# Kernel optimization log

Hardware: AMD Instinct MI355X
Metric: run time of the kernel (lower is better)

Reference implementation:

```python
import jax, jax.numpy as jnp
import numpy as np

NEG_BIG = -9e15  # matches torch's -9000000000000000.0 mask value


def _gat_layer(x, adj_mask, W, a):
    # x: [N, Fin], W: [Fin, Fout], a: [Fout]
    h = x @ W                                   # [N, Fout]
    d = jnp.abs(h[None, :, :] - h[:, None, :])  # [N, N, Fout] pairwise |h_j - h_i|
    e = jax.nn.relu(jnp.einsum('ijf,f->ij', d, a))
    e = jnp.where(adj_mask, e, NEG_BIG)
    att = jax.nn.softmax(e, axis=1)             # row softmax (dropout p=0, skipped)
    return jax.nn.relu(att @ h)


def setup_inputs() -> dict:
    key = jax.random.key(0)
    ks = jax.random.split(key, 10)
    N, F, H, C = 1024, 128, 128, 16

    def xavier(k, shape, gain=1.414):
        fan_in, fan_out = shape[0], shape[-1]
        bound = gain * np.sqrt(6.0 / (fan_in + fan_out))
        return jax.random.uniform(k, shape, jnp.float32, -bound, bound)

    feat = jax.random.normal(ks[0], (N, F), jnp.float32)
    adj = jax.random.randint(ks[1], (N, N), 0, 2, jnp.int32)
    return {
        'feat': feat,
        'adj': adj,
        'W1': xavier(ks[2], (F, H)), 'a1': xavier(ks[3], (H, 1)).squeeze(-1),
        'W2': xavier(ks[4], (H, H)), 'a2': xavier(ks[5], (H, 1)).squeeze(-1),
        'W3': xavier(ks[6], (H, H)), 'a3': xavier(ks[7], (H, 1)).squeeze(-1),
        'Wfc': xavier(ks[8], (H, C), gain=1.0),
        'bfc': jnp.zeros((C,), jnp.float32),
    }


def reference(feat, adj, W1, a1, W2, a2, W3, a3, Wfc, bfc):
    mask = adj > 0
    x = _gat_layer(feat, mask, W1, a1)
    x = _gat_layer(x, mask, W2, a2)
    x = _gat_layer(x, mask, W3, a3)
    # EdgeGCN (include_adj=False): pairwise abs-diff -> linear, output [N*N, C]
    N, H = x.shape
    diff = jnp.abs(x[None, :, :] - x[:, None, :]).reshape(N * N, H)
    return diff @ Wfc + bfc
```

## Files before the change

kernel.cpp:

```cpp
#include <hip/hip_runtime.h>
#include <math.h>

#define NEG_BIG -9.0e15f

typedef __attribute__((ext_vector_type(4))) float f32x4;
typedef __attribute__((ext_vector_type(8))) short bf16x8;
typedef __attribute__((ext_vector_type(4))) unsigned int u32x4;

__global__ __launch_bounds__(128) void gemm_xw_t(const float* __restrict__ X,
                                                 const float* __restrict__ W,
                                                 float* __restrict__ HT) {
  __shared__ float xrow[128];
  const int i = blockIdx.x;
  const int o = threadIdx.x;
  xrow[o] = X[(size_t)i * 128 + o];
  __syncthreads();
  float acc = 0.f;
#pragma unroll 16
  for (int k = 0; k < 128; ++k) acc = fmaf(xrow[k], W[(size_t)k * 128 + o], acc);
  HT[(size_t)o * 1024 + i] = acc;
}

#define ABSFMA4(acc, hv, ha)                        \
  acc.x = fmaf(fabsf(hv.x - ha.x), ha.y, acc.x);    \
  acc.y = fmaf(fabsf(hv.y - ha.x), ha.y, acc.y);    \
  acc.z = fmaf(fabsf(hv.z - ha.x), ha.y, acc.z);    \
  acc.w = fmaf(fabsf(hv.w - ha.x), ha.y, acc.w);

#define DOT4(acc, hv, p) \
  acc = fmaf(hv.x, p.x, fmaf(hv.y, p.y, fmaf(hv.z, p.z, fmaf(hv.w, p.w, acc))));

__global__ __launch_bounds__(1024, 4) void gat_attn(const float* __restrict__ HT,
                                                    const int* __restrict__ adj,
                                                    const float* __restrict__ a,
                                                    float* __restrict__ Xout) {
  __shared__ float ep2[2][4][1024];
  __shared__ float e_s[4][1024];
  __shared__ float2 ha_s[4][128];
  __shared__ float redm[4][4];
  __shared__ float redsum[4][4];
  __shared__ float inv_s[4];

  const int t = threadIdx.x;
  const int i0 = blockIdx.x * 4;
  const float4* __restrict__ HT4 = reinterpret_cast<const float4*>(HT);

  if (t < 512) {
    const int pil = t >> 7;
    const int f = t & 127;
    ha_s[pil][f] = make_float2(HT[(size_t)f * 1024 + i0 + pil], a[f]);
  }
  __syncthreads();

  const int ih = t >> 9;
  const int fh = (t >> 8) & 1;
  const int jt = t & 255;
  const int il = t >> 8;
  const int j0 = (t & 255) * 4;

  float4 esum = {0.f, 0.f, 0.f, 0.f};
#pragma unroll
  for (int pass = 0; pass < 2; ++pass) {
    const int fb = pass * 64 + fh * 32;
    float4 aA = {0.f, 0.f, 0.f, 0.f};
    float4 aB = {0.f, 0.f, 0.f, 0.f};
#pragma unroll 4
    for (int ff = 0; ff < 32; ++ff) {
      const int f = fb + ff;
      const float4 hv = HT4[f * 256 + jt];
      const float2 hA = ha_s[ih * 2][f];
      const float2 hB = ha_s[ih * 2 + 1][f];
      ABSFMA4(aA, hv, hA);
      ABSFMA4(aB, hv, hB);
    }
    *reinterpret_cast<float4*>(&ep2[fh][ih * 2][jt * 4]) = aA;
    *reinterpret_cast<float4*>(&ep2[fh][ih * 2 + 1][jt * 4]) = aB;
    __syncthreads();
    {
      const float4 s0 = *reinterpret_cast<const float4*>(&ep2[0][il][j0]);
      const float4 s1 = *reinterpret_cast<const float4*>(&ep2[1][il][j0]);
      esum.x += s0.x + s1.x;
      esum.y += s0.y + s1.y;
      esum.z += s0.z + s1.z;
      esum.w += s0.w + s1.w;
    }
    __syncthreads();
  }

  float4 e;
  {
    const int4 ad = *reinterpret_cast<const int4*>(&adj[(size_t)(i0 + il) * 1024 + j0]);
    e.x = ad.x > 0 ? fmaxf(esum.x, 0.f) : NEG_BIG;
    e.y = ad.y > 0 ? fmaxf(esum.y, 0.f) : NEG_BIG;
    e.z = ad.z > 0 ? fmaxf(esum.z, 0.f) : NEG_BIG;
    e.w = ad.w > 0 ? fmaxf(esum.w, 0.f) : NEG_BIG;
  }

  const int wq = (t >> 6) & 3;
  float m = fmaxf(fmaxf(e.x, e.y), fmaxf(e.z, e.w));
#pragma unroll
  for (int off = 32; off > 0; off >>= 1) m = fmaxf(m, __shfl_xor(m, off));
  if ((t & 63) == 0) redm[il][wq] = m;
  __syncthreads();
  m = fmaxf(fmaxf(redm[il][0], redm[il][1]), fmaxf(redm[il][2], redm[il][3]));
  float4 p;
  p.x = __expf(e.x - m);
  p.y = __expf(e.y - m);
  p.z = __expf(e.z - m);
  p.w = __expf(e.w - m);
  *reinterpret_cast<float4*>(&e_s[il][j0]) = p;
  float s = p.x + p.y + p.z + p.w;
#pragma unroll
  for (int off = 32; off > 0; off >>= 1) s += __shfl_xor(s, off);
  if ((t & 63) == 0) redsum[il][wq] = s;
  __syncthreads();
  if (t < 4) {
    const float ss = redsum[t][0] + redsum[t][1] + redsum[t][2] + redsum[t][3];
    inv_s[t] = 1.f / ss;
  }
  __syncthreads();

  const int w = t >> 6;
  const int l = t & 63;
  const int f0 = w * 8;
  float acc[8][4];
#pragma unroll
  for (int ff = 0; ff < 8; ++ff)
#pragma unroll
    for (int r = 0; r < 4; ++r) acc[ff][r] = 0.f;

#pragma unroll
  for (int jb = 0; jb < 4; ++jb) {
    const int j4 = jb * 64 + l;
    const float4 p0 = *reinterpret_cast<const float4*>(&e_s[0][j4 * 4]);
    const float4 p1 = *reinterpret_cast<const float4*>(&e_s[1][j4 * 4]);
    const float4 p2 = *reinterpret_cast<const float4*>(&e_s[2][j4 * 4]);
    const float4 p3 = *reinterpret_cast<const float4*>(&e_s[3][j4 * 4]);
#pragma unroll
    for (int ff = 0; ff < 8; ++ff) {
      const float4 hv = HT4[(f0 + ff) * 256 + j4];
      DOT4(acc[ff][0], hv, p0);
      DOT4(acc[ff][1], hv, p1);
      DOT4(acc[ff][2], hv, p2);
      DOT4(acc[ff][3], hv, p3);
    }
  }

  float v[32];
#pragma unroll
  for (int ff = 0; ff < 8; ++ff)
#pragma unroll
    for (int r = 0; r < 4; ++r) v[ff * 4 + r] = acc[ff][r];

#pragma unroll
  for (int step = 0; step < 5; ++step) {
    const int s2 = 1 << step;
    const bool hi = (l & s2) != 0;
#pragma unroll
    for (int k = 0; k < (32 >> (step + 1)); ++k) {
      const float x = v[2 * k];
      const float y = v[2 * k + 1];
      float tt = hi ? x : y;
      tt = __shfl_xor(tt, s2);
      v[k] = (hi ? y : x) + tt;
    }
  }
  float r = v[0] + __shfl_xor(v[0], 32);

  if (l < 32) {
    const int oidx = l & 31;
    const int ff = oidx >> 2;
    const int orow = oidx & 3;
    const float o = fmaxf(r * inv_s[orow], 0.f);
    Xout[(size_t)(i0 + orow) * 128 + f0 + ff] = o;
  }
}

__global__ __launch_bounds__(256) void edge_fc_mfma(const float* __restrict__ X,
                                                    const float* __restrict__ Wfc,
                                                    const float* __restrict__ bfc,
                                                    float* __restrict__ out) {
  __shared__ float xi_s[32][132];
  __shared__ float xj_s[32][132];
  __shared__ float ostage[4][256];

  const int t = threadIdx.x;
  const int bid = blockIdx.x;
  int jb = (int)((sqrtf(8.0f * (float)bid + 1.0f) - 1.0f) * 0.5f);
  int ib = bid - jb * (jb + 1) / 2;
  if (ib > jb) { jb++; ib = bid - jb * (jb + 1) / 2; }
  if (ib < 0) { jb--; ib = bid - jb * (jb + 1) / 2; }

  {
    const int r = t >> 3;
    const int c0 = (t & 7) * 16;
    const float4* gi = reinterpret_cast<const float4*>(X + (size_t)(ib * 32 + r) * 128 + c0);
    const float4* gj = reinterpret_cast<const float4*>(X + (size_t)(jb * 32 + r) * 128 + c0);
#pragma unroll
    for (int k = 0; k < 4; ++k) {
      *reinterpret_cast<float4*>(&xi_s[r][c0 + k * 4]) = gi[k];
      *reinterpret_cast<float4*>(&xj_s[r][c0 + k * 4]) = gj[k];
    }
  }

  const int w = t >> 6, lane = t & 63;
  const int col = lane & 15, kg = lane >> 4;

  bf16x8 bhi[4], blo[4];
#pragma unroll
  for (int c = 0; c < 4; ++c) {
    bf16x8 bh, bl;
#pragma unroll
    for (int j = 0; j < 8; ++j) {
      const float wv = Wfc[(c * 32 + kg * 8 + j) * 16 + col];
      const unsigned u = __builtin_bit_cast(unsigned, wv);
      const unsigned h = u & 0xffff0000u;
      const float lof = wv - __builtin_bit_cast(float, h);
      bh[j] = (short)(h >> 16);
      bl[j] = (short)(__builtin_bit_cast(unsigned, lof) >> 16);
    }
    bhi[c] = bh;
    blo[c] = bl;
  }
  const float bb = bfc[col];

  __syncthreads();

  const int j0 = (w & 1) * 16;
  const int ih = w >> 1;
  unsigned xjr[4][8];
#pragma unroll
  for (int c = 0; c < 4; ++c) {
    const float4 v0 = *reinterpret_cast<const float4*>(&xj_s[j0 + col][c * 32 + kg * 8]);
    const float4 v1 = *reinterpret_cast<const float4*>(&xj_s[j0 + col][c * 32 + kg * 8 + 4]);
    xjr[c][0] = __builtin_bit_cast(unsigned, v0.x);
    xjr[c][1] = __builtin_bit_cast(unsigned, v0.y);
    xjr[c][2] = __builtin_bit_cast(unsigned, v0.z);
    xjr[c][3] = __builtin_bit_cast(unsigned, v0.w);
    xjr[c][4] = __builtin_bit_cast(unsigned, v1.x);
    xjr[c][5] = __builtin_bit_cast(unsigned, v1.y);
    xjr[c][6] = __builtin_bit_cast(unsigned, v1.z);
    xjr[c][7] = __builtin_bit_cast(unsigned, v1.w);
  }

  const bool mirror = (ib != jb);

  for (int i = 0; i < 16; ++i) {
    const int li = ih * 16 + i;
    const int gi = ib * 32 + li;
    f32x4 acc = {bb, bb, bb, bb};
#pragma unroll
    for (int c = 0; c < 4; ++c) {
      const float4 v0 = *reinterpret_cast<const float4*>(&xi_s[li][c * 32 + kg * 8]);
      const float4 v1 = *reinterpret_cast<const float4*>(&xi_s[li][c * 32 + kg * 8 + 4]);
      unsigned xiv[8];
      xiv[0] = __builtin_bit_cast(unsigned, v0.x);
      xiv[1] = __builtin_bit_cast(unsigned, v0.y);
      xiv[2] = __builtin_bit_cast(unsigned, v0.z);
      xiv[3] = __builtin_bit_cast(unsigned, v0.w);
      xiv[4] = __builtin_bit_cast(unsigned, v1.x);
      xiv[5] = __builtin_bit_cast(unsigned, v1.y);
      xiv[6] = __builtin_bit_cast(unsigned, v1.z);
      xiv[7] = __builtin_bit_cast(unsigned, v1.w);
      u32x4 ahv, alv;
#pragma unroll
      for (int q = 0; q < 4; ++q) {
        const float d0 = __builtin_bit_cast(float, xjr[c][2 * q]) -
                         __builtin_bit_cast(float, xiv[2 * q]);
        const float d1 = __builtin_bit_cast(float, xjr[c][2 * q + 1]) -
                         __builtin_bit_cast(float, xiv[2 * q + 1]);
        const unsigned h0 = __builtin_bit_cast(unsigned, d0) & 0x7fff0000u;
        const unsigned h1 = __builtin_bit_cast(unsigned, d1) & 0x7fff0000u;
        const float lo0 = fabsf(d0) - __builtin_bit_cast(float, h0);
        const float lo1 = fabsf(d1) - __builtin_bit_cast(float, h1);
        ahv[q] = __builtin_amdgcn_perm(h1, h0, 0x07060302u);
        alv[q] = __builtin_amdgcn_perm(__builtin_bit_cast(unsigned, lo1),
                                       __builtin_bit_cast(unsigned, lo0), 0x07060302u);
      }
      const bf16x8 ah = __builtin_bit_cast(bf16x8, ahv);
      const bf16x8 al = __builtin_bit_cast(bf16x8, alv);
      acc = __builtin_amdgcn_mfma_f32_16x16x32_bf16(ah, bhi[c], acc, 0, 0, 0);
      acc = __builtin_amdgcn_mfma_f32_16x16x32_bf16(ah, blo[c], acc, 0, 0, 0);
      acc = __builtin_amdgcn_mfma_f32_16x16x32_bf16(al, bhi[c], acc, 0, 0, 0);
    }
#pragma unroll
    for (int r = 0; r < 4; ++r) ostage[w][(kg * 4 + r) * 16 + col] = acc[r];
    const f32x4 vv = *reinterpret_cast<const f32x4*>(&ostage[w][lane * 4]);
    const int jl = lane >> 2;
    const int c0 = (lane & 3) * 4;
    const int gj = jb * 32 + j0 + jl;
    __builtin_nontemporal_store(vv, reinterpret_cast<f32x4*>(out + ((size_t)gi * 1024 + gj) * 16 + c0));
    if (mirror)
      __builtin_nontemporal_store(vv, reinterpret_cast<f32x4*>(out + ((size_t)gj * 1024 + gi) * 16 + c0));
  }
}

extern "C" void kernel_launch(void* const* d_in, const int* in_sizes, int n_in,
                              void* d_out, int out_size, void* d_ws, size_t ws_size,
                              hipStream_t stream) {
  const float* feat = (const float*)d_in[0];
  const int* adj = (const int*)d_in[1];
  const float* W1 = (const float*)d_in[2];
  const float* a1 = (const float*)d_in[3];
  const float* W2 = (const float*)d_in[4];
  const float* a2 = (const float*)d_in[5];
  const float* W3 = (const float*)d_in[6];
  const float* a3 = (const float*)d_in[7];
  const float* Wfc = (const float*)d_in[8];
  const float* bfc = (const float*)d_in[9];
  float* out = (float*)d_out;

  float* ht = (float*)d_ws;
  float* xA = ht + 131072;
  float* xB = xA + 131072;

  gemm_xw_t<<<1024, 128, 0, stream>>>(feat, W1, ht);
  gat_attn<<<256, 1024, 0, stream>>>(ht, adj, a1, xA);
  gemm_xw_t<<<1024, 128, 0, stream>>>(xA, W2, ht);
  gat_attn<<<256, 1024, 0, stream>>>(ht, adj, a2, xB);
  gemm_xw_t<<<1024, 128, 0, stream>>>(xB, W3, ht);
  gat_attn<<<256, 1024, 0, stream>>>(ht, adj, a3, xA);
  edge_fc_mfma<<<528, 256, 0, stream>>>(xA, Wfc, bfc, out);
}
```

Measured before the change: 106.6 us.

## Split edge FC blocks into quarters and precompute bf16 hi/lo weight split

The edge FC kernel now launches four times as many blocks, each handling 8 rows of the i-tile instead of 32, so more blocks are in flight for the store-bound output write. The bf16 hi/lo split of Wfc moves into a tiny one-block kernel that writes pre-packed vectors to workspace, so each edge block loads them directly instead of recomputing. The cost is that each xj tile is reloaded four times and there is one more kernel launch.

Result: slower. 111.4 us (+4.4%).

```diff
diff --git a/kernel.cpp b/kernel.cpp
--- a/kernel.cpp
+++ b/kernel.cpp
@@ -176,58 +176,77 @@
   }
 }
 
+__global__ __launch_bounds__(256) void split_wfc(const float* __restrict__ Wfc,
+                                                 u32x4* __restrict__ hi,
+                                                 u32x4* __restrict__ lo) {
+  const int t = threadIdx.x;
+  const int col = t & 15, kg = (t >> 4) & 3, c = t >> 6;
+  unsigned hs[8], ls[8];
+#pragma unroll
+  for (int j = 0; j < 8; ++j) {
+    const float wv = Wfc[(c * 32 + kg * 8 + j) * 16 + col];
+    const unsigned u = __builtin_bit_cast(unsigned, wv);
+    const unsigned h = u & 0xffff0000u;
+    hs[j] = h;
+    ls[j] = __builtin_bit_cast(unsigned, wv - __builtin_bit_cast(float, h));
+  }
+  u32x4 hv, lv;
+#pragma unroll
+  for (int q = 0; q < 4; ++q) {
+    hv[q] = __builtin_amdgcn_perm(hs[2 * q + 1], hs[2 * q], 0x07060302u);
+    lv[q] = __builtin_amdgcn_perm(ls[2 * q + 1], ls[2 * q], 0x07060302u);
+  }
+  hi[t] = hv;
+  lo[t] = lv;
+}
+
 __global__ __launch_bounds__(256) void edge_fc_mfma(const float* __restrict__ X,
-                                                    const float* __restrict__ Wfc,
+                                                    const u32x4* __restrict__ whi,
+                                                    const u32x4* __restrict__ wlo,
                                                     const float* __restrict__ bfc,
                                                     float* __restrict__ out) {
-  __shared__ float xi_s[32][132];
-  __shared__ float xj_s[32][132];
+  __shared__ float xj_s[32][128];
+  __shared__ float xi_s[8][128];
   __shared__ float ostage[4][256];
 
   const int t = threadIdx.x;
-  const int bid = blockIdx.x;
-  int jb = (int)((sqrtf(8.0f * (float)bid + 1.0f) - 1.0f) * 0.5f);
-  int ib = bid - jb * (jb + 1) / 2;
-  if (ib > jb) { jb++; ib = bid - jb * (jb + 1) / 2; }
-  if (ib < 0) { jb--; ib = bid - jb * (jb + 1) / 2; }
+  const int tid2 = blockIdx.x >> 2;
+  const int q = blockIdx.x & 3;
+  int jb = (int)((sqrtf(8.0f * (float)tid2 + 1.0f) - 1.0f) * 0.5f);
+  int ib = tid2 - jb * (jb + 1) / 2;
+  if (ib > jb) { jb++; ib = tid2 - jb * (jb + 1) / 2; }
+  if (ib < 0) { jb--; ib = tid2 - jb * (jb + 1) / 2; }
 
   {
     const int r = t >> 3;
     const int c0 = (t & 7) * 16;
-    const float4* gi = reinterpret_cast<const float4*>(X + (size_t)(ib * 32 + r) * 128 + c0);
     const float4* gj = reinterpret_cast<const float4*>(X + (size_t)(jb * 32 + r) * 128 + c0);
 #pragma unroll
-    for (int k = 0; k < 4; ++k) {
-      *reinterpret_cast<float4*>(&xi_s[r][c0 + k * 4]) = gi[k];
-      *reinterpret_cast<float4*>(&xj_s[r][c0 + k * 4]) = gj[k];
+    for (int k = 0; k < 4; ++k) *reinterpret_cast<float4*>(&xj_s[r][c0 + k * 4]) = gj[k];
+    if (t < 64) {
+      const float4* gi = reinterpret_cast<const float4*>(
+          X + (size_t)(ib * 32 + q * 8 + (t >> 3)) * 128 + c0);
+#pragma unroll
+      for (int k = 0; k < 4; ++k)
+        *reinterpret_cast<float4*>(&xi_s[t >> 3][c0 + k * 4]) = gi[k];
     }
   }
 
   const int w = t >> 6, lane = t & 63;
   const int col = lane & 15, kg = lane >> 4;
+  const int is = w >> 1, j0 = (w & 1) * 16;
 
   bf16x8 bhi[4], blo[4];
 #pragma unroll
   for (int c = 0; c < 4; ++c) {
-    bf16x8 bh, bl;
-#pragma unroll
-    for (int j = 0; j < 8; ++j) {
-      const float wv = Wfc[(c * 32 + kg * 8 + j) * 16 + col];
-      const unsigned u = __builtin_bit_cast(unsigned, wv);
-      const unsigned h = u & 0xffff0000u;
-      const float lof = wv - __builtin_bit_cast(float, h);
-      bh[j] = (short)(h >> 16);
-      bl[j] = (short)(__builtin_bit_cast(unsigned, lof) >> 16);
-    }
-    bhi[c] = bh;
-    blo[c] = bl;
+    const int fi = c * 64 + kg * 16 + col;
+    bhi[c] = __builtin_bit_cast(bf16x8, whi[fi]);
+    blo[c] = __builtin_bit_cast(bf16x8, wlo[fi]);
   }
   const float bb = bfc[col];
 
   __syncthreads();
 
-  const int j0 = (w & 1) * 16;
-  const int ih = w >> 1;
   unsigned xjr[4][8];
 #pragma unroll
   for (int c = 0; c < 4; ++c) {
@@ -245,9 +264,9 @@
 
   const bool mirror = (ib != jb);
 
-  for (int i = 0; i < 16; ++i) {
-    const int li = ih * 16 + i;
-    const int gi = ib * 32 + li;
+  for (int i = 0; i < 4; ++i) {
+    const int li = is * 4 + i;
+    const int gi = ib * 32 + q * 8 + li;
     f32x4 acc = {bb, bb, bb, bb};
 #pragma unroll
     for (int c = 0; c < 4; ++c) {
@@ -264,18 +283,18 @@
       xiv[7] = __builtin_bit_cast(unsigned, v1.w);
       u32x4 ahv, alv;
 #pragma unroll
-      for (int q = 0; q < 4; ++q) {
-        const float d0 = __builtin_bit_cast(float, xjr[c][2 * q]) -
-                         __builtin_bit_cast(float, xiv[2 * q]);
-        const float d1 = __builtin_bit_cast(float, xjr[c][2 * q + 1]) -
-                         __builtin_bit_cast(float, xiv[2 * q + 1]);
+      for (int qq = 0; qq < 4; ++qq) {
+        const float d0 = __builtin_bit_cast(float, xjr[c][2 * qq]) -
+                         __builtin_bit_cast(float, xiv[2 * qq]);
+        const float d1 = __builtin_bit_cast(float, xjr[c][2 * qq + 1]) -
+                         __builtin_bit_cast(float, xiv[2 * qq + 1]);
         const unsigned h0 = __builtin_bit_cast(unsigned, d0) & 0x7fff0000u;
         const unsigned h1 = __builtin_bit_cast(unsigned, d1) & 0x7fff0000u;
         const float lo0 = fabsf(d0) - __builtin_bit_cast(float, h0);
         const float lo1 = fabsf(d1) - __builtin_bit_cast(float, h1);
-        ahv[q] = __builtin_amdgcn_perm(h1, h0, 0x07060302u);
-        alv[q] = __builtin_amdgcn_perm(__builtin_bit_cast(unsigned, lo1),
-                                       __builtin_bit_cast(unsigned, lo0), 0x07060302u);
+        ahv[qq] = __builtin_amdgcn_perm(h1, h0, 0x07060302u);
+        alv[qq] = __builtin_amdgcn_perm(__builtin_bit_cast(unsigned, lo1),
+                                        __builtin_bit_cast(unsigned, lo0), 0x07060302u);
       }
       const bf16x8 ah = __builtin_bit_cast(bf16x8, ahv);
       const bf16x8 al = __builtin_bit_cast(bf16x8, alv);
@@ -313,12 +332,15 @@
   float* ht = (float*)d_ws;
   float* xA = ht + 131072;
   float* xB = xA + 131072;
-
+  u32x4* whi = (u32x4*)(xB + 131072);
+  u32x4* wlo = whi + 256;
+
+  split_wfc<<<1, 256, 0, stream>>>(Wfc, whi, wlo);
   gemm_xw_t<<<1024, 128, 0, stream>>>(feat, W1, ht);
   gat_attn<<<256, 1024, 0, stream>>>(ht, adj, a1, xA);
   gemm_xw_t<<<1024, 128, 0, stream>>>(xA, W2, ht);
   gat_attn<<<256, 1024, 0, stream>>>(ht, adj, a2, xB);
   gemm_xw_t<<<1024, 128, 0, stream>>>(xB, W3, ht);
   gat_attn<<<256, 1024, 0, stream>>>(ht, adj, a3, xA);
-  edge_fc_mfma<<<528, 256, 0, stream>>>(xA, Wfc, bfc, out);
-}
+  edge_fc_mfma<<<2112, 256, 0, stream>>>(xA, whi, wlo, bfc, out);
+}
```
